# Kernel optimization log

Measured on AMD Instinct MI355X. Metric: run time of the kernel, lower is better.

The kernel has to match this reference:

```python
import jax, jax.numpy as jnp
import numpy as np

B, D_IN, D_H, D_OUT = 8192, 512, 256, 128
TEMP = 0.07
EPS_BN = 1e-5


def _bn(x, g, b):
    # BatchNorm1d in training mode: biased batch statistics
    mu = jnp.mean(x, axis=0)
    var = jnp.var(x, axis=0)
    return (x - mu) * jax.lax.rsqrt(var + EPS_BN) * g + b


def _project(x, W1, b1, g1, beta1, W2, b2, g2, beta2, W3, b3):
    h = jax.nn.relu(_bn(x @ W1 + b1, g1, beta1))
    h = jax.nn.relu(_bn(h @ W2 + b2, g2, beta2))
    return h @ W3 + b3  # (B, D_OUT)


def setup_inputs() -> dict:
    key = jax.random.key(0)
    ks = jax.random.split(key, 6)
    f32 = jnp.float32
    return {
        "x1": jax.random.normal(ks[0], (B, D_IN), f32),
        "x2": jax.random.normal(ks[1], (B, D_IN), f32),
        "W1": jax.random.normal(ks[2], (D_IN, D_H), f32) * 0.04,
        "b1": jnp.zeros((D_H,), f32),
        "g1": jnp.ones((D_H,), f32),
        "beta1": jnp.zeros((D_H,), f32),
        "W2": jax.random.normal(ks[3], (D_H, D_H), f32) * 0.06,
        "b2": jnp.zeros((D_H,), f32),
        "g2": jnp.ones((D_H,), f32),
        "beta2": jnp.zeros((D_H,), f32),
        "W3": jax.random.normal(ks[4], (D_H, D_OUT), f32) * 0.06,
        "b3": jnp.zeros((D_OUT,), f32),
    }


def reference(x1, x2, W1, b1, g1, beta1, W2, b2, g2, beta2, W3, b3):
    z1 = _project(x1, W1, b1, g1, beta1, W2, b2, g2, beta2, W3, b3)
    z2 = _project(x2, W1, b1, g1, beta1, W2, b2, g2, beta2, W3, b3)
    # F.normalize(dim=1), eps=1e-12
    z1 = z1 / jnp.maximum(jnp.linalg.norm(z1, axis=1, keepdims=True), 1e-12)
    z2 = z2 / jnp.maximum(jnp.linalg.norm(z2, axis=1, keepdims=True), 1e-12)
    reps = jnp.concatenate([z1, z2], axis=0)           # (2B, D)
    # cosine similarity of unit vectors == single GEMM (2B, 2B)
    sim = reps @ reps.T
    idx = jnp.arange(B)
    positives = jnp.concatenate([sim[idx, idx + B], sim[idx + B, idx]], axis=0)  # (2B,)
    nominator = jnp.exp(positives / TEMP)
    # source bug preserved: denominator sums sim/temp (no exp), masking the diagonal
    denominator = (jnp.sum(sim, axis=1) - jnp.diagonal(sim)) / TEMP
    loss = -jnp.log(nominator / denominator)
    return jnp.mean(loss)
```

## Files before the change

kernel.cpp:

```cpp
#include <hip/hip_runtime.h>
#include <math.h>

#define BATCH   8192
#define MROWS   16384
#define DIN     512
#define DH      256
#define DOUT    128
#define EPS_BN  1e-5f
#define TEMP    0.07f

using f4    = __attribute__((ext_vector_type(4))) float;
using f32x4 = __attribute__((ext_vector_type(4))) float;
using h4    = __attribute__((ext_vector_type(4))) _Float16;
using h8    = __attribute__((ext_vector_type(8))) _Float16;

#define GLD_LDS16(gp, lp) __builtin_amdgcn_global_load_lds( \
    (const __attribute__((address_space(1))) void*)(gp),    \
    (__attribute__((address_space(3))) void*)(lp), 16, 0, 0)

template <int K, int N, int FUSE_BN, int EPI>
__global__ __launch_bounds__(256, 2) void gemm_fused(
    const float* __restrict__ A1, const float* __restrict__ A2, int splitRow,
    const _Float16* __restrict__ BThi, const _Float16* __restrict__ BTlo,
    const float* __restrict__ stats, const float* __restrict__ g,
    const float* __restrict__ beta, const float* __restrict__ bias,
    float* __restrict__ Cout, float* __restrict__ red)
{
    constexpr int NT = K / 32;

    const int tid = threadIdx.x;
    const int wave = tid >> 6, lane = tid & 63;
    const int wr = wave >> 1, wc = wave & 1;
    const int l4 = lane >> 4, lc = lane & 15;
    const int wg = blockIdx.x;
    const int brow = (wg & 255) * 64;
    const int bcol = (wg >> 8) * 128;
    const int half = (brow >= BATCH) ? 1 : 0;

    __shared__ __align__(16) char smem[75776];
    _Float16* Bring = (_Float16*)smem;
    _Float16* Aring = (_Float16*)(smem + 49152);
    float*    scsh  = (float*)(smem + 73728);
    float*    sR    = (float*)(smem + 49152);
    float*    nLp   = (float*)(smem + 49152 + 8192);

    const _Float16* bsrc[4];
    {
        const int co = (bcol + wave * 32 + lc) * K + l4 * 8;
        bsrc[0] = BThi + co;
        bsrc[1] = BThi + co + 16 * K;
        bsrc[2] = BTlo + co;
        bsrc[3] = BTlo + co + 16 * K;
    }
    auto stageB = [&](int buf, int t) {
        _Float16* d = Bring + buf * 8192 + wave * 1024;
        GLD_LDS16(bsrc[0] + t * 32, d);
        GLD_LDS16(bsrc[1] + t * 32, d + 512);
        GLD_LDS16(bsrc[2] + t * 32, d + 4096);
        GLD_LDS16(bsrc[3] + t * 32, d + 4096 + 512);
    };

    const int arow = wave * 16 + lc;
    const int ak0 = l4 * 8;
    const int growA = brow + arow;
    const float* asrc = (growA < splitRow)
        ? (A1 + (size_t)growA * K + ak0)
        : (A2 + (size_t)(growA - splitRow) * K + ak0);

    f4 ar[2][2];
    auto loadA = [&](int p, int t) {
        ar[p][0] = *(const f4*)(asrc + t * 32);
        ar[p][1] = *(const f4*)(asrc + t * 32 + 4);
    };
    auto procA = [&](int p, int buf, int t) {
        float v[8];
#pragma unroll
        for (int j = 0; j < 4; ++j) { v[j] = ar[p][0][j]; v[4 + j] = ar[p][1][j]; }
        if constexpr (FUSE_BN) {
            f4 s0 = *(const f4*)&scsh[t * 32 + ak0];
            f4 s1 = *(const f4*)&scsh[t * 32 + ak0 + 4];
            f4 h0 = *(const f4*)&scsh[256 + t * 32 + ak0];
            f4 h1 = *(const f4*)&scsh[256 + t * 32 + ak0 + 4];
#pragma unroll
            for (int j = 0; j < 4; ++j) {
                v[j]     = fmaxf(fmaf(v[j],     s0[j], h0[j]), 0.f);
                v[4 + j] = fmaxf(fmaf(v[4 + j], s1[j], h1[j]), 0.f);
            }
        }
        h8 hi, lo;
#pragma unroll
        for (int j = 0; j < 8; ++j) {
            _Float16 h = (_Float16)v[j];
            hi[j] = h;
            lo[j] = (_Float16)(v[j] - (float)h);
        }
        _Float16* d = Aring + buf * 4096 + wave * 512 + lane * 8;
        *(h8*)d = hi;
        *(h8*)(d + 2048) = lo;
    };

    f32x4 acc[2][4];
#pragma unroll
    for (int mi = 0; mi < 2; ++mi)
#pragma unroll
        for (int ni = 0; ni < 4; ++ni)
#pragma unroll
            for (int c = 0; c < 4; ++c) acc[mi][ni][c] = 0.f;

    auto compute = [&](int buf) {
        const _Float16* Ab = Aring + buf * 4096;
        const _Float16* Bb = Bring + buf * 8192;
        h8 ah[2], al[2], bh[4], bl[4];
#pragma unroll
        for (int mi = 0; mi < 2; ++mi) {
            ah[mi] = *(const h8*)(Ab + (wr * 2 + mi) * 512 + lane * 8);
            al[mi] = *(const h8*)(Ab + 2048 + (wr * 2 + mi) * 512 + lane * 8);
        }
#pragma unroll
        for (int ni = 0; ni < 4; ++ni) {
            bh[ni] = *(const h8*)(Bb + (wc * 4 + ni) * 512 + lane * 8);
            bl[ni] = *(const h8*)(Bb + 4096 + (wc * 4 + ni) * 512 + lane * 8);
        }
#pragma unroll
        for (int mi = 0; mi < 2; ++mi)
#pragma unroll
            for (int ni = 0; ni < 4; ++ni) {
                acc[mi][ni] = __builtin_amdgcn_mfma_f32_16x16x32_f16(
                    ah[mi], bh[ni], acc[mi][ni], 0, 0, 0);
                acc[mi][ni] = __builtin_amdgcn_mfma_f32_16x16x32_f16(
                    al[mi], bh[ni], acc[mi][ni], 0, 0, 0);
                acc[mi][ni] = __builtin_amdgcn_mfma_f32_16x16x32_f16(
                    ah[mi], bl[ni], acc[mi][ni], 0, 0, 0);
            }
    };

    if constexpr (FUSE_BN) {
        const float invN = 1.0f / (float)BATCH;
        float mu = stats[half * 512 + tid] * invN;
        float var = fmaf(-mu, mu, stats[half * 512 + 256 + tid] * invN);
        float s = g[tid] * rsqrtf(var + EPS_BN);
        scsh[tid] = s;
        scsh[256 + tid] = fmaf(-mu, s, beta[tid]);
    }
    loadA(0, 0);
    stageB(0, 0);
    stageB(1, 1);
    if constexpr (FUSE_BN) {
        asm volatile("s_waitcnt lgkmcnt(0)" ::: "memory");
        __builtin_amdgcn_s_barrier();
    }
    procA(0, 0, 0);
    loadA(1, 1);
    asm volatile("s_waitcnt vmcnt(6)" ::: "memory");
    asm volatile("s_waitcnt lgkmcnt(0)" ::: "memory");
    __builtin_amdgcn_s_barrier();

#pragma unroll
    for (int t = 0; t < NT; ++t) {
        if (t + 2 < NT) stageB((t + 2) % 3, t + 2);
        compute(t % 3);
        if (t + 1 < NT) {
            if (t + 2 < NT) asm volatile("s_waitcnt vmcnt(4)" ::: "memory");
            else            asm volatile("s_waitcnt vmcnt(0)" ::: "memory");
            __builtin_amdgcn_sched_barrier(0);
            procA((t + 1) & 1, (t + 1) % 3, t + 1);
            if (t + 2 < NT) loadA(t & 1, t + 2);
        }
        asm volatile("s_waitcnt lgkmcnt(0)" ::: "memory");
        __builtin_amdgcn_s_barrier();
    }
    __syncthreads();

    float bv[4];
#pragma unroll
    for (int ni = 0; ni < 4; ++ni) bv[ni] = bias[bcol + wc * 64 + ni * 16 + lc];

    if constexpr (EPI == 0) {
        float s[4] = {}, q[4] = {};
#pragma unroll
        for (int mi = 0; mi < 2; ++mi)
#pragma unroll
            for (int j = 0; j < 4; ++j) {
                int gr = brow + wr * 32 + mi * 16 + l4 * 4 + j;
#pragma unroll
                for (int ni = 0; ni < 4; ++ni) {
                    float v = acc[mi][ni][j] + bv[ni];
                    Cout[(size_t)gr * N + bcol + wc * 64 + ni * 16 + lc] = v;
                    s[ni] += v;
                    q[ni] = fmaf(v, v, q[ni]);
                }
            }
#pragma unroll
        for (int ni = 0; ni < 4; ++ni) {
            sR[(wr * 4 + l4) * 128 + wc * 64 + ni * 16 + lc] = s[ni];
            sR[1024 + (wr * 4 + l4) * 128 + wc * 64 + ni * 16 + lc] = q[ni];
        }
        __syncthreads();
        if (tid < 128) {
            float ss = 0.f, qq = 0.f;
#pragma unroll
            for (int i = 0; i < 8; ++i) {
                ss += sR[i * 128 + tid];
                qq += sR[1024 + i * 128 + tid];
            }
            atomicAdd(&red[half * 512 + bcol + tid], ss);
            atomicAdd(&red[half * 512 + 256 + bcol + tid], qq);
        }
    } else {
        float v[2][4][4];
#pragma unroll
        for (int mi = 0; mi < 2; ++mi)
#pragma unroll
            for (int j = 0; j < 4; ++j) {
                float ssq = 0.f;
#pragma unroll
                for (int ni = 0; ni < 4; ++ni) {
                    v[mi][j][ni] = acc[mi][ni][j] + bv[ni];
                    ssq = fmaf(v[mi][j][ni], v[mi][j][ni], ssq);
                }
#pragma unroll
                for (int o = 1; o < 16; o <<= 1) ssq += __shfl_xor(ssq, o);
                if (lc == 0) nLp[(wr * 32 + mi * 16 + l4 * 4 + j) * 2 + wc] = ssq;
            }
        __syncthreads();
        float s[4] = {};
#pragma unroll
        for (int mi = 0; mi < 2; ++mi)
#pragma unroll
            for (int j = 0; j < 4; ++j) {
                int lrow = wr * 32 + mi * 16 + l4 * 4 + j;
                float tot = nLp[lrow * 2] + nLp[lrow * 2 + 1];
                float inv = 1.0f / fmaxf(sqrtf(tot), 1e-12f);
#pragma unroll
                for (int ni = 0; ni < 4; ++ni) {
                    float z = v[mi][j][ni] * inv;
                    Cout[(size_t)(brow + lrow) * DOUT + wc * 64 + ni * 16 + lc] = z;
                    s[ni] += z;
                }
            }
        __syncthreads();
#pragma unroll
        for (int ni = 0; ni < 4; ++ni)
            sR[(wr * 4 + l4) * 128 + wc * 64 + ni * 16 + lc] = s[ni];
        __syncthreads();
        if (tid < 128) {
            float ss = 0.f;
#pragma unroll
            for (int i = 0; i < 8; ++i) ss += sR[i * 128 + tid];
            atomicAdd(&red[tid], ss);
        }
    }
}

__global__ __launch_bounds__(256) void wprep(
    const float* __restrict__ W1, const float* __restrict__ W2,
    const float* __restrict__ W3,
    _Float16* __restrict__ W1hiT, _Float16* __restrict__ W1loT,
    _Float16* __restrict__ W2hiT, _Float16* __restrict__ W2loT,
    _Float16* __restrict__ W3hiT, _Float16* __restrict__ W3loT,
    float* __restrict__ smalls, float* __restrict__ out)
{
    const int b = blockIdx.x;
    if (b == 56) {
        for (int i = threadIdx.x; i < 2176; i += 256) smalls[i] = 0.f;
        if (threadIdx.x == 0) out[0] = 0.f;
        return;
    }
#pragma unroll
    for (int i = 0; i < 4; ++i) {
        int qd = b * 1024 + i * 256 + threadIdx.x;
        const float* src; _Float16 *dhi, *dlo; int n, kq, Nw, Kw;
        if (qd < 32768)      { src = W1; dhi = W1hiT; dlo = W1loT;
                               n = qd & 255;            kq = qd >> 8; Nw = 256; Kw = 512; }
        else if (qd < 49152) { src = W2; dhi = W2hiT; dlo = W2loT;
                               n = (qd - 32768) & 255;  kq = (qd - 32768) >> 8; Nw = 256; Kw = 256; }
        else                 { src = W3; dhi = W3hiT; dlo = W3loT;
                               n = (qd - 49152) & 127;  kq = (qd - 49152) >> 7; Nw = 128; Kw = 256; }
        h4 hi, lo;
#pragma unroll
        for (int j = 0; j < 4; ++j) {
            float w = src[(size_t)(kq * 4 + j) * Nw + n];
            _Float16 h = (_Float16)w;
            hi[j] = h;
            lo[j] = (_Float16)(w - (float)h);
        }
        *(h4*)&dhi[(size_t)n * Kw + kq * 4] = hi;
        *(h4*)&dlo[(size_t)n * Kw + kq * 4] = lo;
    }
}

__global__ __launch_bounds__(256) void losspos(const float* __restrict__ reps,
                                               const float* __restrict__ Svec,
                                               float* __restrict__ out)
{
    const int lane = threadIdx.x & 63;
    const int grp = threadIdx.x >> 6;
    __shared__ float part[4];
    float2 sv = ((const float2*)Svec)[lane];
    float acc = 0.f;
#pragma unroll 1
    for (int it = 0; it < 8; ++it) {
        int p = blockIdx.x * 32 + it * 4 + grp;
        float2 a = ((const float2*)(reps + (size_t)p * DOUT))[lane];
        float2 b = ((const float2*)(reps + (size_t)(p + BATCH) * DOUT))[lane];
        float dp  = fmaf(a.x, b.x, a.y * b.y);
        float rsA = fmaf(a.x, sv.x, a.y * sv.y);
        float sdA = fmaf(a.x, a.x, a.y * a.y);
        float rsB = fmaf(b.x, sv.x, b.y * sv.y);
        float sdB = fmaf(b.x, b.x, b.y * b.y);
#pragma unroll
        for (int o = 32; o; o >>= 1) {
            dp  += __shfl_xor(dp, o);
            rsA += __shfl_xor(rsA, o);
            sdA += __shfl_xor(sdA, o);
            rsB += __shfl_xor(rsB, o);
            sdB += __shfl_xor(sdB, o);
        }
        if (lane == 0) {
            float nom = expf(dp / TEMP);
            float dA = (rsA - sdA) / TEMP;
            float dB = (rsB - sdB) / TEMP;
            acc += -logf(nom / dA) - logf(nom / dB);
        }
    }
    if (lane == 0) part[grp] = acc;
    __syncthreads();
    if (threadIdx.x == 0) {
        float t = part[0] + part[1] + part[2] + part[3];
        atomicAdd(out, t * (1.0f / (float)MROWS));
    }
}

extern "C" void kernel_launch(void* const* d_in, const int* in_sizes, int n_in,
                              void* d_out, int out_size, void* d_ws, size_t ws_size,
                              hipStream_t stream)
{
    const float* x1    = (const float*)d_in[0];
    const float* x2    = (const float*)d_in[1];
    const float* W1    = (const float*)d_in[2];
    const float* b1    = (const float*)d_in[3];
    const float* g1    = (const float*)d_in[4];
    const float* beta1 = (const float*)d_in[5];
    const float* W2    = (const float*)d_in[6];
    const float* b2    = (const float*)d_in[7];
    const float* g2    = (const float*)d_in[8];
    const float* beta2 = (const float*)d_in[9];
    const float* W3    = (const float*)d_in[10];
    const float* b3    = (const float*)d_in[11];
    float* out = (float*)d_out;

    char* W = (char*)d_ws;
    float*    Y1   = (float*)(W);
    float*    Y2   = (float*)(W + (16u << 20));
    float*    REPS = (float*)(W + (32u << 20));
    char* wb = W + (40u << 20);
    _Float16* W1HIT = (_Float16*)(wb);
    _Float16* W1LOT = (_Float16*)(wb + 262144);
    _Float16* W2HIT = (_Float16*)(wb + 524288);
    _Float16* W2LOT = (_Float16*)(wb + 655360);
    _Float16* W3HIT = (_Float16*)(wb + 786432);
    _Float16* W3LOT = (_Float16*)(wb + 851968);
    float* smalls   = (float*)  (wb + 917504);
    float* stats1 = smalls;
    float* stats2 = smalls + 1024;
    float* Svec   = smalls + 2048;

    const int big = 1 << 30;

    wprep<<<57, 256, 0, stream>>>(W1, W2, W3, W1HIT, W1LOT, W2HIT, W2LOT,
                                  W3HIT, W3LOT, smalls, out);

    gemm_fused<DIN, DH, 0, 0><<<512, 256, 0, stream>>>(
        x1, x2, BATCH, W1HIT, W1LOT, nullptr, nullptr, nullptr, b1, Y1, stats1);

    gemm_fused<DH, DH, 1, 0><<<512, 256, 0, stream>>>(
        Y1, Y1, big, W2HIT, W2LOT, stats1, g1, beta1, b2, Y2, stats2);

    gemm_fused<DH, DOUT, 1, 1><<<256, 256, 0, stream>>>(
        Y2, Y2, big, W3HIT, W3LOT, stats2, g2, beta2, b3, REPS, Svec);

    losspos<<<BATCH / 32, 256, 0, stream>>>(REPS, Svec, out);
}
```

Before: 166.7 us.

## Deepen A-prefetch to three stages, raise MFMA priority, split loss over more blocks

The A-operand register prefetch becomes a three-deep ring, loading two tiles ahead with adjusted vmcnt waits so global latency is hidden across more compute. BN stats loads are issued before the A/B prefetches, and the scale/shift math runs after them, so those loads overlap. s_setprio raises wave priority around the MFMA block. The loss kernel processes 16 rows per block over 512 blocks instead of 32 over 256, for more parallelism. The cost is extra VGPRs for the third A buffer, which could pressure occupancy at launch_bounds(256,2).

```diff
diff --git a/kernel.cpp b/kernel.cpp
--- a/kernel.cpp
+++ b/kernel.cpp
@@ -17,6 +17,9 @@
 #define GLD_LDS16(gp, lp) __builtin_amdgcn_global_load_lds( \
     (const __attribute__((address_space(1))) void*)(gp),    \
     (__attribute__((address_space(3))) void*)(lp), 16, 0, 0)
+
+#define VMCNT(n) asm volatile("s_waitcnt vmcnt(" #n ")" ::: "memory")
+#define LGKM0()  asm volatile("s_waitcnt lgkmcnt(0)" ::: "memory")
 
 template <int K, int N, int FUSE_BN, int EPI>
 __global__ __launch_bounds__(256, 2) void gemm_fused(
@@ -67,7 +70,7 @@
         ? (A1 + (size_t)growA * K + ak0)
         : (A2 + (size_t)(growA - splitRow) * K + ak0);
 
-    f4 ar[2][2];
+    f4 ar[3][2];
     auto loadA = [&](int p, int t) {
         ar[p][0] = *(const f4*)(asrc + t * 32);
         ar[p][1] = *(const f4*)(asrc + t * 32 + 4);
@@ -121,6 +124,7 @@
             bh[ni] = *(const h8*)(Bb + (wc * 4 + ni) * 512 + lane * 8);
             bl[ni] = *(const h8*)(Bb + 4096 + (wc * 4 + ni) * 512 + lane * 8);
         }
+        __builtin_amdgcn_s_setprio(1);
 #pragma unroll
         for (int mi = 0; mi < 2; ++mi)
 #pragma unroll
@@ -132,27 +136,35 @@
                 acc[mi][ni] = __builtin_amdgcn_mfma_f32_16x16x32_f16(
                     ah[mi], bl[ni], acc[mi][ni], 0, 0, 0);
             }
+        __builtin_amdgcn_s_setprio(0);
     };
 
+    float st0, st1, gv, bt;
     if constexpr (FUSE_BN) {
-        const float invN = 1.0f / (float)BATCH;
-        float mu = stats[half * 512 + tid] * invN;
-        float var = fmaf(-mu, mu, stats[half * 512 + 256 + tid] * invN);
-        float s = g[tid] * rsqrtf(var + EPS_BN);
-        scsh[tid] = s;
-        scsh[256 + tid] = fmaf(-mu, s, beta[tid]);
+        st0 = stats[half * 512 + tid];
+        st1 = stats[half * 512 + 256 + tid];
+        gv = g[tid];
+        bt = beta[tid];
     }
     loadA(0, 0);
+    loadA(1, 1);
+    loadA(2, 2);
     stageB(0, 0);
     stageB(1, 1);
     if constexpr (FUSE_BN) {
-        asm volatile("s_waitcnt lgkmcnt(0)" ::: "memory");
+        const float invN = 1.0f / (float)BATCH;
+        float mu = st0 * invN;
+        float var = fmaf(-mu, mu, st1 * invN);
+        float s = gv * rsqrtf(var + EPS_BN);
+        scsh[tid] = s;
+        scsh[256 + tid] = fmaf(-mu, s, bt);
+        LGKM0();
         __builtin_amdgcn_s_barrier();
     }
     procA(0, 0, 0);
-    loadA(1, 1);
-    asm volatile("s_waitcnt vmcnt(6)" ::: "memory");
-    asm volatile("s_waitcnt lgkmcnt(0)" ::: "memory");
+    loadA(0, 3);
+    VMCNT(6);
+    LGKM0();
     __builtin_amdgcn_s_barrier();
 
 #pragma unroll
@@ -160,13 +172,14 @@
         if (t + 2 < NT) stageB((t + 2) % 3, t + 2);
         compute(t % 3);
         if (t + 1 < NT) {
-            if (t + 2 < NT) asm volatile("s_waitcnt vmcnt(4)" ::: "memory");
-            else            asm volatile("s_waitcnt vmcnt(0)" ::: "memory");
+            if (t + 3 < NT)      VMCNT(6);
+            else if (t + 2 < NT) VMCNT(4);
+            else                 VMCNT(0);
             __builtin_amdgcn_sched_barrier(0);
-            procA((t + 1) & 1, (t + 1) % 3, t + 1);
-            if (t + 2 < NT) loadA(t & 1, t + 2);
-        }
-        asm volatile("s_waitcnt lgkmcnt(0)" ::: "memory");
+            procA((t + 1) % 3, (t + 1) % 3, t + 1);
+            if (t + 4 < NT) loadA((t + 4) % 3, t + 4);
+        }
+        LGKM0();
         __builtin_amdgcn_s_barrier();
     }
     __syncthreads();
@@ -299,8 +312,8 @@
     float2 sv = ((const float2*)Svec)[lane];
     float acc = 0.f;
 #pragma unroll 1
-    for (int it = 0; it < 8; ++it) {
-        int p = blockIdx.x * 32 + it * 4 + grp;
+    for (int it = 0; it < 4; ++it) {
+        int p = blockIdx.x * 16 + it * 4 + grp;
         float2 a = ((const float2*)(reps + (size_t)p * DOUT))[lane];
         float2 b = ((const float2*)(reps + (size_t)(p + BATCH) * DOUT))[lane];
         float dp  = fmaf(a.x, b.x, a.y * b.y);
@@ -379,5 +392,5 @@
     gemm_fused<DH, DOUT, 1, 1><<<256, 256, 0, stream>>>(
         Y2, Y2, big, W3HIT, W3LOT, stats2, g2, beta2, b3, REPS, Svec);
 
-    losspos<<<BATCH / 32, 256, 0, stream>>>(REPS, Svec, out);
+    losspos<<<512, 256, 0, stream>>>(REPS, Svec, out);
 }
```

After: 169.0 us. Within noise of the previous version (+1.4%).
